# Kernel tuning notes

Measured on AMD Instinct MI355X. Metric: run time of the kernel, lower is better.

Reference implementation:

```python
import jax, jax.numpy as jnp
import numpy as np

D_MODEL = 2048
N_HEADS = 16
D_K = D_MODEL // N_HEADS
BATCH = 2
SEQ = 2048


def _rope(q, k):
    # q,k: [B, H, S, Dk], interleaved even/odd RoPE as in the torch source
    seq_len = q.shape[2]
    d = q.shape[-1]
    freqs = 1.0 / (10000.0 ** (jnp.arange(0, d, 2.0, dtype=jnp.float32) / d))  # [Dk/2]
    pos = jnp.arange(seq_len, dtype=jnp.float32)
    ang = pos[:, None] * freqs[None, :]          # [S, Dk/2]
    sin, cos = jnp.sin(ang), jnp.cos(ang)

    def rot(t):
        te, to = t[..., ::2], t[..., 1::2]
        out = jnp.stack([te * cos - to * sin, te * sin + to * cos], axis=-1)
        return out.reshape(t.shape)

    return rot(q), rot(k)


def setup_inputs() -> dict:
    key = jax.random.key(0)
    ks = jax.random.split(key, 5)
    scale = 1.0 / np.sqrt(D_MODEL)
    return {
        "x": jax.random.normal(ks[0], (BATCH, SEQ, D_MODEL), jnp.float32),
        "w_q": jax.random.normal(ks[1], (D_MODEL, D_MODEL), jnp.float32) * scale,
        "w_k": jax.random.normal(ks[2], (D_MODEL, D_MODEL), jnp.float32) * scale,
        "w_v": jax.random.normal(ks[3], (D_MODEL, D_MODEL), jnp.float32) * scale,
        "w_o": jax.random.normal(ks[4], (D_MODEL, D_MODEL), jnp.float32) * scale,
        "b_o": jnp.zeros((D_MODEL,), jnp.float32),
    }


def reference(x, w_q, w_k, w_v, w_o, b_o):
    B, S, D = x.shape
    H, Dk = N_HEADS, D_K
    # nn.Linear: y = x @ W.T
    q = (x @ w_q.T).reshape(B, S, H, Dk).transpose(0, 2, 1, 3)
    k = (x @ w_k.T).reshape(B, S, H, Dk).transpose(0, 2, 1, 3)
    v = (x @ w_v.T).reshape(B, S, H, Dk).transpose(0, 2, 1, 3)
    q, k = _rope(q, k)
    scores = jnp.einsum('bhqd,bhkd->bhqk', q, k) / jnp.sqrt(jnp.float32(Dk))
    causal = jnp.tril(jnp.ones((S, S), bool))  # True = keep
    scores = jnp.where(causal[None, None], scores, -jnp.inf)
    attn = jax.nn.softmax(scores, axis=-1)
    out = jnp.einsum('bhqk,bhkd->bhqd', attn, v)
    out = out.transpose(0, 2, 1, 3).reshape(B, S, D)
    return out @ w_o.T + b_o
```

## Files before the change

kernel.cpp:

```cpp
#include <hip/hip_runtime.h>

#define D_MODEL 2048
#define NHEADS  16
#define DK      128
#define BATCH   2
#define SEQ     2048
#define MTOT    (BATCH*SEQ)

typedef unsigned short u16;
typedef unsigned int   u32;
typedef __bf16 bf16x8 __attribute__((ext_vector_type(8)));
typedef float  f32x4  __attribute__((ext_vector_type(4)));

__device__ __forceinline__ float b2f(u16 u) {
  return __uint_as_float(((u32)u) << 16);
}
__device__ __forceinline__ u16 f2b(float f) {
  u32 x = __float_as_uint(f);
  x += 0x7fffu + ((x >> 16) & 1u);
  return (u16)(x >> 16);
}

__device__ __forceinline__ void gl2lds16(const u16* g, u16* l) {
  __builtin_amdgcn_global_load_lds(
      (const __attribute__((address_space(1))) void*)g,
      (__attribute__((address_space(3))) void*)l, 16, 0, 0);
}

__global__ __launch_bounds__(256) void cvt_k(const float* __restrict__ in,
                                             u16* __restrict__ out, int n4) {
  int i = blockIdx.x * 256 + threadIdx.x;
  if (i >= n4) return;
  float4 v = ((const float4*)in)[i];
  u32 lo = (u32)f2b(v.x) | ((u32)f2b(v.y) << 16);
  u32 hi = (u32)f2b(v.z) | ((u32)f2b(v.w) << 16);
  ((uint2*)out)[i] = make_uint2(lo, hi);
}

__global__ __launch_bounds__(256) void cvt4_k(const float* __restrict__ a, const float* __restrict__ b,
                                              const float* __restrict__ c, const float* __restrict__ d,
                                              u16* __restrict__ oa, u16* __restrict__ ob,
                                              u16* __restrict__ oc, u16* __restrict__ od, int n4) {
  int z = blockIdx.y;
  const float* in = (z == 0) ? a : (z == 1) ? b : (z == 2) ? c : d;
  u16* out = (z == 0) ? oa : (z == 1) ? ob : (z == 2) ? oc : od;
  int i = blockIdx.x * 256 + threadIdx.x;
  if (i >= n4) return;
  float4 v = ((const float4*)in)[i];
  u32 lo = (u32)f2b(v.x) | ((u32)f2b(v.y) << 16);
  u32 hi = (u32)f2b(v.z) | ((u32)f2b(v.w) << 16);
  ((uint2*)out)[i] = make_uint2(lo, hi);
}

__global__ __launch_bounds__(512, 2) void gemm256(const u16* __restrict__ A,
                                                  const u16* __restrict__ B,
                                                  const int M, const int N, const int K,
                                                  u16* __restrict__ outb,
                                                  float* __restrict__ outf,
                                                  const float* __restrict__ bias,
                                                  const int mode) {
  __shared__ __align__(16) u16 smem[65536];

  const int t    = threadIdx.x;
  const int lane = t & 63;
  const int wave = t >> 6;
  const int wm   = wave >> 2, wn = wave & 3;
  const int quad = lane >> 4, l16 = lane & 15;
  const int m0 = blockIdx.y * 256, n0 = blockIdx.x * 256;
  const int sr = lane & 15, sc = lane >> 4;

  const u16* aSrc[4]; u32 aDst[4];
  const u16* bSrc[4]; u32 bDst[4];
#pragma unroll
  for (int q = 0; q < 4; ++q) {
    int id = q * 8 + wave;
    int kc = id >> 4, t16 = id & 15;
    aSrc[q] = A + (size_t)(m0 + t16 * 16 + sr) * K + kc * 32 + sc * 8;
    aDst[q] = (u32)id * 512;
    bSrc[q] = B + (size_t)(n0 + t16 * 16 + sr) * K + kc * 32 + sc * 8;
    bDst[q] = 16384u + (u32)id * 512;
  }

  f32x4 acc[8][4] = {};
  const int NT = K >> 6;

#pragma unroll
  for (int q = 0; q < 4; ++q) {
    gl2lds16(aSrc[q], smem + aDst[q]); aSrc[q] += 64;
    gl2lds16(bSrc[q], smem + bDst[q]); bSrc[q] += 64;
  }

  for (int tt = 0; tt < NT; ++tt) {
    u16* bufC = smem + (tt & 1) * 32768;
    u16* bufN = smem + ((tt & 1) ^ 1) * 32768;
    const bool more = (tt + 1 < NT);

    if (more) {
      gl2lds16(aSrc[0], bufN + aDst[0]); aSrc[0] += 64;
      gl2lds16(bSrc[0], bufN + bDst[0]); bSrc[0] += 64;
      asm volatile("s_waitcnt vmcnt(2)" ::: "memory");
    } else {
      asm volatile("s_waitcnt vmcnt(0)" ::: "memory");
    }
    __builtin_amdgcn_s_barrier();

    const u16* Ab = bufC;
    const u16* Bb = bufC + 16384;
    bf16x8 af[4], bfv[4];

#pragma unroll
    for (int ii = 0; ii < 4; ++ii)
      af[ii] = *(const bf16x8*)&Ab[(u32)(wm * 8 + ii) * 512 + lane * 8];
#pragma unroll
    for (int j = 0; j < 4; ++j)
      bfv[j] = *(const bf16x8*)&Bb[(u32)(wn * 4 + j) * 512 + lane * 8];
    if (more) {
      gl2lds16(aSrc[1], bufN + aDst[1]); aSrc[1] += 64;
      gl2lds16(bSrc[1], bufN + bDst[1]); bSrc[1] += 64;
      gl2lds16(aSrc[2], bufN + aDst[2]); aSrc[2] += 64;
      gl2lds16(bSrc[2], bufN + bDst[2]); bSrc[2] += 64;
    }
    __builtin_amdgcn_s_barrier();
    asm volatile("s_waitcnt lgkmcnt(0)" ::: "memory");
    __builtin_amdgcn_s_setprio(1);
#pragma unroll
    for (int ii = 0; ii < 4; ++ii)
#pragma unroll
      for (int j = 0; j < 4; ++j)
        acc[ii][j] = __builtin_amdgcn_mfma_f32_16x16x32_bf16(af[ii], bfv[j], acc[ii][j], 0, 0, 0);
    __builtin_amdgcn_s_setprio(0);
    __builtin_amdgcn_s_barrier();

#pragma unroll
    for (int ii = 0; ii < 4; ++ii)
      af[ii] = *(const bf16x8*)&Ab[(u32)(wm * 8 + 4 + ii) * 512 + lane * 8];
    if (more) {
      gl2lds16(aSrc[3], bufN + aDst[3]); aSrc[3] += 64;
      gl2lds16(bSrc[3], bufN + bDst[3]); bSrc[3] += 64;
    }
    __builtin_amdgcn_s_barrier();
    asm volatile("s_waitcnt lgkmcnt(0)" ::: "memory");
    __builtin_amdgcn_s_setprio(1);
#pragma unroll
    for (int ii = 0; ii < 4; ++ii)
#pragma unroll
      for (int j = 0; j < 4; ++j)
        acc[ii + 4][j] = __builtin_amdgcn_mfma_f32_16x16x32_bf16(af[ii], bfv[j], acc[ii + 4][j], 0, 0, 0);
    __builtin_amdgcn_s_setprio(0);
    __builtin_amdgcn_s_barrier();

#pragma unroll
    for (int ii = 0; ii < 4; ++ii)
      af[ii] = *(const bf16x8*)&Ab[(u32)(16 + wm * 8 + ii) * 512 + lane * 8];
#pragma unroll
    for (int j = 0; j < 4; ++j)
      bfv[j] = *(const bf16x8*)&Bb[(u32)(16 + wn * 4 + j) * 512 + lane * 8];
    __builtin_amdgcn_s_barrier();
    asm volatile("s_waitcnt lgkmcnt(0)" ::: "memory");
    __builtin_amdgcn_s_setprio(1);
#pragma unroll
    for (int ii = 0; ii < 4; ++ii)
#pragma unroll
      for (int j = 0; j < 4; ++j)
        acc[ii][j] = __builtin_amdgcn_mfma_f32_16x16x32_bf16(af[ii], bfv[j], acc[ii][j], 0, 0, 0);
    __builtin_amdgcn_s_setprio(0);
    __builtin_amdgcn_s_barrier();

#pragma unroll
    for (int ii = 0; ii < 4; ++ii)
      af[ii] = *(const bf16x8*)&Ab[(u32)(16 + wm * 8 + 4 + ii) * 512 + lane * 8];
    __builtin_amdgcn_s_barrier();
    asm volatile("s_waitcnt lgkmcnt(0)" ::: "memory");
    __builtin_amdgcn_s_setprio(1);
#pragma unroll
    for (int ii = 0; ii < 4; ++ii)
#pragma unroll
      for (int j = 0; j < 4; ++j)
        acc[ii + 4][j] = __builtin_amdgcn_mfma_f32_16x16x32_bf16(af[ii], bfv[j], acc[ii + 4][j], 0, 0, 0);
    __builtin_amdgcn_s_setprio(0);
    __builtin_amdgcn_s_barrier();
  }

  if (mode == 0) {
#pragma unroll
    for (int i = 0; i < 8; ++i)
#pragma unroll
      for (int j = 0; j < 4; ++j)
#pragma unroll
        for (int rr = 0; rr < 4; ++rr) {
          int row = m0 + wm * 128 + i * 16 + quad * 4 + rr;
          int col = n0 + wn * 64 + j * 16 + l16;
          outf[(size_t)row * N + col] = acc[i][j][rr] + bias[col];
        }
  } else {
    const int hcol = n0 + wn * 64;
    const int tens = hcol >> 11;
    const int h    = (hcol >> 7) & 15;
    const int db   = hcol & 127;
    const bool doRope = (tens < 2);
    const float mult = (tens == 0) ? 0.08838834764831845f : 1.0f;
#pragma unroll
    for (int j = 0; j < 4; ++j) {
      const int d = db + j * 16 + l16;
      const float freq = exp2f(-0.20762050593045951f * (float)(d >> 1));
      const float sgn  = (d & 1) ? 1.f : -1.f;
#pragma unroll
      for (int i = 0; i < 8; ++i)
#pragma unroll
        for (int rr = 0; rr < 4; ++rr) {
          int row = m0 + wm * 128 + i * 16 + quad * 4 + rr;
          int b = row >> 11;
          int s = row & (SEQ - 1);
          float v = acc[i][j][rr];
          if (doRope) {
            float sn, cs;
            __sincosf((float)s * freq, &sn, &cs);
            float pv = __shfl_xor(v, 1);
            v = (v * cs + sgn * pv * sn) * mult;
          }
          outb[(size_t)tens * 8388608 + (((size_t)(b * NHEADS + h)) * SEQ + s) * DK + d] = f2b(v);
        }
    }
  }
}

__global__ __launch_bounds__(256) void vt_k(const u16* __restrict__ V,
                                            u16* __restrict__ Vt) {
  constexpr int LDT = 72;
  __shared__ __align__(16) u16 tile[64 * LDT];
  const int s0 = blockIdx.x * 64, d0 = blockIdx.y * 64, bh = blockIdx.z;
  const u16* in = V + (size_t)bh * SEQ * DK;
  u16* out = Vt + (size_t)bh * DK * SEQ;
  const int t = threadIdx.x;
  const int r = t >> 3, cg = t & 7;
#pragma unroll
  for (int half = 0; half < 2; ++half) {
    uint4 v = *(const uint4*)(in + (size_t)(s0 + r + half * 32) * DK + d0 + cg * 8);
    *(uint4*)&tile[(r + half * 32) * LDT + cg * 8] = v;
  }
  __syncthreads();
#pragma unroll
  for (int half = 0; half < 2; ++half) {
    int d = (t >> 3) + half * 32;
    __align__(16) u16 tmp[8];
#pragma unroll
    for (int i = 0; i < 8; ++i) tmp[i] = tile[(cg * 8 + i) * LDT + d];
    *(uint4*)(out + (size_t)(d0 + d) * SEQ + s0 + cg * 8) = *(const uint4*)tmp;
  }
}

__global__ __launch_bounds__(256, 4) void attn_k(const u16* __restrict__ Q,
                                                 const u16* __restrict__ K,
                                                 const u16* __restrict__ Vt,
                                                 u16* __restrict__ out) {
  __shared__ __align__(16) u16 smem[8192 + 8192 + 4096];
  u16* Ks = smem;
  u16* Vs = smem + 8192;

  const int t    = threadIdx.x;
  const int lane = t & 63;
  const int wave = t >> 6;
  const int quad = lane >> 4, l16 = lane & 15;
  u16* Psw = smem + 16384 + wave * 1024;
  const int pmask = (l16 & 7) << 3;
  const int qt = (int)gridDim.x - 1 - (int)blockIdx.x;
  const int bh = blockIdx.y;
  const size_t baseQK = (size_t)bh * SEQ * DK;
  const size_t baseV  = (size_t)bh * DK * SEQ;
  const int qw = qt * 64 + wave * 16;
  const int qglob = qw + l16;

  bf16x8 qf[4];
#pragma unroll
  for (int kc = 0; kc < 4; ++kc)
    qf[kc] = *(const bf16x8*)(Q + baseQK + (size_t)(qw + l16) * DK + kc * 32 + quad * 8);

  f32x4 oacc[8] = {};
  float m_run = -1e30f, l_run = 0.f;

  const int sr = lane & 15, sc = lane >> 4;
  const u16* kp[4]; u16* kd[4];
  const u16* vp[4]; u16* vd[4];
#pragma unroll
  for (int j = 0; j < 4; ++j) {
    int lin = wave * 4 + j;
    int knt = lin >> 2, kkc = lin & 3;
    kp[j] = K + baseQK + (size_t)(knt * 16 + sr) * DK + kkc * 32 + sc * 8;
    kd[j] = Ks + lin * 512;
    int vkc = lin >> 3, vnt = lin & 7;
    vp[j] = Vt + baseV + (size_t)(vnt * 16 + sr) * SEQ + vkc * 32 + sc * 8;
    vd[j] = Vs + lin * 512;
  }

  const int kend = (qt + 1) * 64;
  for (int k0 = 0; k0 < kend; k0 += 64) {
    __syncthreads();
#pragma unroll
    for (int j = 0; j < 4; ++j) gl2lds16(kp[j], kd[j]);
#pragma unroll
    for (int j = 0; j < 4; ++j) gl2lds16(vp[j], vd[j]);
#pragma unroll
    for (int j = 0; j < 4; ++j) { kp[j] += (size_t)64 * DK; vp[j] += 64; }
    __syncthreads();

    if (k0 >= qw + 16) continue;

    f32x4 s[4] = {};
#pragma unroll
    for (int kc = 0; kc < 4; ++kc) {
#pragma unroll
      for (int nt = 0; nt < 4; ++nt) {
        bf16x8 kf = *(const bf16x8*)&Ks[(nt * 4 + kc) * 512 + lane * 8];
        s[nt] = __builtin_amdgcn_mfma_f32_16x16x32_bf16(kf, qf[kc], s[nt], 0, 0, 0);
      }
    }

    float p[4][4];
    float newm = m_run;
    if (k0 + 63 > qw) {
#pragma unroll
      for (int nt = 0; nt < 4; ++nt)
#pragma unroll
        for (int r = 0; r < 4; ++r) {
          int key = k0 + nt * 16 + quad * 4 + r;
          float v = (key <= qglob) ? s[nt][r] : -1e30f;
          p[nt][r] = v;
          newm = fmaxf(newm, v);
        }
    } else {
#pragma unroll
      for (int nt = 0; nt < 4; ++nt)
#pragma unroll
        for (int r = 0; r < 4; ++r) {
          p[nt][r] = s[nt][r];
          newm = fmaxf(newm, s[nt][r]);
        }
    }
    newm = fmaxf(newm, __shfl_xor(newm, 16));
    newm = fmaxf(newm, __shfl_xor(newm, 32));
    float lsum = 0.f;
#pragma unroll
    for (int nt = 0; nt < 4; ++nt)
#pragma unroll
      for (int r = 0; r < 4; ++r) {
        float e = __expf(p[nt][r] - newm);
        p[nt][r] = e;
        lsum += e;
      }
    lsum += __shfl_xor(lsum, 16);
    lsum += __shfl_xor(lsum, 32);
    float alpha = __expf(m_run - newm);
    l_run = l_run * alpha + lsum;
    m_run = newm;

#pragma unroll
    for (int nt = 0; nt < 4; ++nt) {
      u32 lo = (u32)f2b(p[nt][0]) | ((u32)f2b(p[nt][1]) << 16);
      u32 hi = (u32)f2b(p[nt][2]) | ((u32)f2b(p[nt][3]) << 16);
      *(uint2*)&Psw[l16 * 64 + ((nt * 16 + quad * 4) ^ pmask)] = make_uint2(lo, hi);
    }

#pragma unroll
    for (int r = 0; r < 4; ++r) {
      float av = __shfl(alpha, quad * 4 + r);
#pragma unroll
      for (int nt = 0; nt < 8; ++nt) oacc[nt][r] *= av;
    }

#pragma unroll
    for (int kcp = 0; kcp < 2; ++kcp) {
      bf16x8 pf = *(const bf16x8*)&Psw[l16 * 64 + ((kcp * 32 + quad * 8) ^ pmask)];
#pragma unroll
      for (int nt = 0; nt < 8; ++nt) {
        bf16x8 vf = *(const bf16x8*)&Vs[(kcp * 8 + nt) * 512 + lane * 8];
        oacc[nt] = __builtin_amdgcn_mfma_f32_16x16x32_bf16(pf, vf, oacc[nt], 0, 0, 0);
      }
    }
  }

  constexpr int LDO = 136;
  float invl = 1.f / l_run;
  __syncthreads();
#pragma unroll
  for (int r = 0; r < 4; ++r) {
    float iv = __shfl(invl, quad * 4 + r);
#pragma unroll
    for (int nt = 0; nt < 8; ++nt)
      smem[(wave * 16 + quad * 4 + r) * LDO + nt * 16 + l16] = f2b(oacc[nt][r] * iv);
  }
  __syncthreads();
  const int b = bh >> 4, h = bh & 15;
#pragma unroll
  for (int pss = 0; pss < 4; ++pss) {
    int row = (t >> 4) + pss * 16;
    uint4 v = *(const uint4*)&smem[row * LDO + (t & 15) * 8];
    *(uint4*)(out + ((size_t)(b * SEQ + qt * 64 + row)) * D_MODEL + h * DK + (t & 15) * 8) = v;
  }
}

extern "C" void kernel_launch(void* const* d_in, const int* in_sizes, int n_in,
                              void* d_out, int out_size, void* d_ws, size_t ws_size,
                              hipStream_t stream) {
  const float* x  = (const float*)d_in[0];
  const float* wq = (const float*)d_in[1];
  const float* wk = (const float*)d_in[2];
  const float* wv = (const float*)d_in[3];
  const float* wo = (const float*)d_in[4];
  const float* bo = (const float*)d_in[5];
  float* out = (float*)d_out;

  char* wsb = (char*)d_ws;
  u16* xb    = (u16*)(wsb + 0);
  u16* wqb   = (u16*)(wsb + 16777216);
  u16* wkb   = (u16*)(wsb + 25165824);
  u16* wvb   = (u16*)(wsb + 33554432);
  u16* wob   = (u16*)(wsb + 41943040);
  u16* Qb    = (u16*)(wsb + 50331648);
  u16* Kb    = (u16*)(wsb + 67108864);
  u16* Vb    = (u16*)(wsb + 83886080);
  u16* attnb = xb;
  u16* Vtb   = wqb;

  cvt_k<<<8192, 256, 0, stream>>>(x, xb, MTOT * D_MODEL / 4);
  cvt4_k<<<dim3(4096, 4), 256, 0, stream>>>(wq, wk, wv, wo, wqb, wkb, wvb, wob,
                                            D_MODEL * D_MODEL / 4);

  gemm256<<<dim3(24, 16), 512, 0, stream>>>(xb, wqb, MTOT, 3 * D_MODEL, D_MODEL,
                                            Qb, nullptr, nullptr, 1);

  vt_k<<<dim3(SEQ / 64, DK / 64, BATCH * NHEADS), 256, 0, stream>>>(Vb, Vtb);

  attn_k<<<dim3(SEQ / 64, BATCH * NHEADS), 256, 0, stream>>>(Qb, Kb, Vtb, attnb);

  gemm256<<<dim3(8, 16), 512, 0, stream>>>(attnb, wob, MTOT, D_MODEL, D_MODEL,
                                           nullptr, out, bo, 0);
}
```

Baseline: 532.3 us.

## Simplify GEMM main loop pipeline and add XCD-aware workgroup remapping

Issues all eight global-to-LDS loads for the next tile at the start of each iteration and drops the interleaved barrier/waitcnt choreography in favour of a plain loop over k-chunks with one barrier at the end. It also remaps workgroup IDs so consecutive blocks on the same XCD share A/B rows, aiming for better L2 reuse. The goal is to cut barrier overhead and improve cache locality, at the cost of less fine-grained overlap of loads with MFMA. The remap also assumes the block count is divisible by eight.

Result: slower. 545.2 us (+2.4%).

```diff
diff --git a/kernel.cpp b/kernel.cpp
--- a/kernel.cpp
+++ b/kernel.cpp
@@ -66,7 +66,12 @@
   const int wave = t >> 6;
   const int wm   = wave >> 2, wn = wave & 3;
   const int quad = lane >> 4, l16 = lane & 15;
-  const int m0 = blockIdx.y * 256, n0 = blockIdx.x * 256;
+
+  const int nwg  = (int)(gridDim.x * gridDim.y);
+  const int orig = (int)(blockIdx.y * gridDim.x + blockIdx.x);
+  const int wgid = (orig & 7) * (nwg >> 3) + (orig >> 3);
+  const int bx = wgid % (int)gridDim.x, by = wgid / (int)gridDim.x;
+  const int m0 = by * 256, n0 = bx * 256;
   const int sr = lane & 15, sc = lane >> 4;
 
   const u16* aSrc[4]; u32 aDst[4];
@@ -96,9 +101,12 @@
     const bool more = (tt + 1 < NT);
 
     if (more) {
-      gl2lds16(aSrc[0], bufN + aDst[0]); aSrc[0] += 64;
-      gl2lds16(bSrc[0], bufN + bDst[0]); bSrc[0] += 64;
-      asm volatile("s_waitcnt vmcnt(2)" ::: "memory");
+#pragma unroll
+      for (int q = 0; q < 4; ++q) {
+        gl2lds16(aSrc[q], bufN + aDst[q]); aSrc[q] += 64;
+        gl2lds16(bSrc[q], bufN + bDst[q]); bSrc[q] += 64;
+      }
+      asm volatile("s_waitcnt vmcnt(8)" ::: "memory");
     } else {
       asm volatile("s_waitcnt vmcnt(0)" ::: "memory");
     }
@@ -106,78 +114,28 @@
 
     const u16* Ab = bufC;
     const u16* Bb = bufC + 16384;
-    bf16x8 af[4], bfv[4];
-
-#pragma unroll
-    for (int ii = 0; ii < 4; ++ii)
-      af[ii] = *(const bf16x8*)&Ab[(u32)(wm * 8 + ii) * 512 + lane * 8];
-#pragma unroll
-    for (int j = 0; j < 4; ++j)
-      bfv[j] = *(const bf16x8*)&Bb[(u32)(wn * 4 + j) * 512 + lane * 8];
-    if (more) {
-      gl2lds16(aSrc[1], bufN + aDst[1]); aSrc[1] += 64;
-      gl2lds16(bSrc[1], bufN + bDst[1]); bSrc[1] += 64;
-      gl2lds16(aSrc[2], bufN + aDst[2]); aSrc[2] += 64;
-      gl2lds16(bSrc[2], bufN + bDst[2]); bSrc[2] += 64;
-    }
-    __builtin_amdgcn_s_barrier();
-    asm volatile("s_waitcnt lgkmcnt(0)" ::: "memory");
-    __builtin_amdgcn_s_setprio(1);
-#pragma unroll
-    for (int ii = 0; ii < 4; ++ii)
+#pragma unroll
+    for (int kc = 0; kc < 2; ++kc) {
+      bf16x8 bfv[4];
 #pragma unroll
       for (int j = 0; j < 4; ++j)
-        acc[ii][j] = __builtin_amdgcn_mfma_f32_16x16x32_bf16(af[ii], bfv[j], acc[ii][j], 0, 0, 0);
-    __builtin_amdgcn_s_setprio(0);
-    __builtin_amdgcn_s_barrier();
-
-#pragma unroll
-    for (int ii = 0; ii < 4; ++ii)
-      af[ii] = *(const bf16x8*)&Ab[(u32)(wm * 8 + 4 + ii) * 512 + lane * 8];
-    if (more) {
-      gl2lds16(aSrc[3], bufN + aDst[3]); aSrc[3] += 64;
-      gl2lds16(bSrc[3], bufN + bDst[3]); bSrc[3] += 64;
-    }
-    __builtin_amdgcn_s_barrier();
-    asm volatile("s_waitcnt lgkmcnt(0)" ::: "memory");
-    __builtin_amdgcn_s_setprio(1);
-#pragma unroll
-    for (int ii = 0; ii < 4; ++ii)
-#pragma unroll
-      for (int j = 0; j < 4; ++j)
-        acc[ii + 4][j] = __builtin_amdgcn_mfma_f32_16x16x32_bf16(af[ii], bfv[j], acc[ii + 4][j], 0, 0, 0);
-    __builtin_amdgcn_s_setprio(0);
-    __builtin_amdgcn_s_barrier();
-
-#pragma unroll
-    for (int ii = 0; ii < 4; ++ii)
-      af[ii] = *(const bf16x8*)&Ab[(u32)(16 + wm * 8 + ii) * 512 + lane * 8];
-#pragma unroll
-    for (int j = 0; j < 4; ++j)
-      bfv[j] = *(const bf16x8*)&Bb[(u32)(16 + wn * 4 + j) * 512 + lane * 8];
-    __builtin_amdgcn_s_barrier();
-    asm volatile("s_waitcnt lgkmcnt(0)" ::: "memory");
-    __builtin_amdgcn_s_setprio(1);
-#pragma unroll
-    for (int ii = 0; ii < 4; ++ii)
-#pragma unroll
-      for (int j = 0; j < 4; ++j)
-        acc[ii][j] = __builtin_amdgcn_mfma_f32_16x16x32_bf16(af[ii], bfv[j], acc[ii][j], 0, 0, 0);
-    __builtin_amdgcn_s_setprio(0);
-    __builtin_amdgcn_s_barrier();
-
-#pragma unroll
-    for (int ii = 0; ii < 4; ++ii)
-      af[ii] = *(const bf16x8*)&Ab[(u32)(16 + wm * 8 + 4 + ii) * 512 + lane * 8];
-    __builtin_amdgcn_s_barrier();
-    asm volatile("s_waitcnt lgkmcnt(0)" ::: "memory");
-    __builtin_amdgcn_s_setprio(1);
-#pragma unroll
-    for (int ii = 0; ii < 4; ++ii)
-#pragma unroll
-      for (int j = 0; j < 4; ++j)
-        acc[ii + 4][j] = __builtin_amdgcn_mfma_f32_16x16x32_bf16(af[ii], bfv[j], acc[ii + 4][j], 0, 0, 0);
-    __builtin_amdgcn_s_setprio(0);
+        bfv[j] = *(const bf16x8*)&Bb[(u32)(kc * 16 + wn * 4 + j) * 512 + lane * 8];
+#pragma unroll
+      for (int ih = 0; ih < 2; ++ih) {
+        bf16x8 af[4];
+#pragma unroll
+        for (int ii = 0; ii < 4; ++ii)
+          af[ii] = *(const bf16x8*)&Ab[(u32)(kc * 16 + wm * 8 + ih * 4 + ii) * 512 + lane * 8];
+        __builtin_amdgcn_s_setprio(1);
+#pragma unroll
+        for (int ii = 0; ii < 4; ++ii)
+#pragma unroll
+          for (int j = 0; j < 4; ++j)
+            acc[ih * 4 + ii][j] =
+                __builtin_amdgcn_mfma_f32_16x16x32_bf16(af[ii], bfv[j], acc[ih * 4 + ii][j], 0, 0, 0);
+        __builtin_amdgcn_s_setprio(0);
+      }
+    }
     __builtin_amdgcn_s_barrier();
   }
 
```
